# Kernel tuning notes

Measured on AMD Instinct MI355X. Metric: run time of the kernel, lower is better.

## Reference

```python
import jax, jax.numpy as jnp
import numpy as np

B, C, D = 32768, 1000, 512
ALPHA, BETA = 1.0, 1.0
TEMPERATURE = 0.1


def setup_inputs() -> dict:
    key = jax.random.key(0)
    k1, k2, k3, k4 = jax.random.split(key, 4)
    return {
        "features_front": jax.random.normal(k1, (B, D), dtype=jnp.float32),
        "logits": jax.random.normal(k2, (B, C), dtype=jnp.float32),
        "labels": jax.random.randint(k3, (B,), 0, C, dtype=jnp.int64),
        "text_prototype": jax.random.normal(k4, (C, D), dtype=jnp.float32),
    }


def reference(features_front, logits, labels, text_prototype):
    num_class = text_prototype.shape[0]

    # F.cross_entropy (mean reduction)
    logp = jax.nn.log_softmax(logits, axis=-1)
    loss_ce = -jnp.mean(jnp.take_along_axis(logp, labels[:, None], axis=1)[:, 0])

    # F.normalize(prototypes, dim=1)
    norm = jnp.linalg.norm(text_prototype, axis=1, keepdims=True)
    prototypes = text_prototype / jnp.maximum(norm, 1e-12)

    # supervised contrastive term against class prototypes
    feat_dot_prototype = (features_front @ prototypes.T) / TEMPERATURE  # [B, C]
    logits_max = jax.lax.stop_gradient(jnp.max(feat_dot_prototype, axis=1, keepdims=True))
    lg = feat_dot_prototype - logits_max
    log_prob = lg - jnp.log(jnp.sum(jnp.exp(lg), axis=1, keepdims=True))
    mask = (labels[:, None] == jnp.arange(num_class)[None, :]).astype(log_prob.dtype)
    mean_log_prob_pos = jnp.sum(mask * log_prob, axis=1)
    simloss = -jnp.mean(mean_log_prob_pos)

    # prototype repulsion: sum_{i != j} exp(p_i . p_j) == masked exp-sum of Gram matrix
    gram = prototypes @ prototypes.T  # [C, C]
    offdiag = 1.0 - jnp.eye(num_class, dtype=gram.dtype)
    textloss = jnp.log(jnp.sum(jnp.exp(gram) * offdiag)) / num_class

    return ALPHA * simloss + BETA * loss_ce + textloss
```

## Files before the change

kernel.cpp:

```cpp
#include <hip/hip_runtime.h>
#include <math.h>

#define NB 32768
#define NC 1000
#define ND 512
#define NTILES 63
#define LOG2E 1.4426950408889634f
#define LN2 0.6931471805599453f
#define S2 14.426950408889634f
#define NBUCKET 64

typedef __attribute__((ext_vector_type(8))) short short8;
typedef __attribute__((ext_vector_type(4))) float f32x4;

__device__ __forceinline__ float fexp2(float x) {
    float r; asm("v_exp_f32 %0, %1" : "=v"(r) : "v"(x)); return r;
}
__device__ __forceinline__ float flog2(float x) {
    float r; asm("v_log_f32 %0, %1" : "=v"(r) : "v"(x)); return r;
}
__device__ __forceinline__ unsigned short bf16_rne(float f) {
    unsigned int u = __builtin_bit_cast(unsigned int, f);
    u += 0x7FFFu + ((u >> 16) & 1u);
    return (unsigned short)(u >> 16);
}
__device__ __forceinline__ short8 pack8f(float4 a, float4 b) {
    short8 s;
    s[0] = (short)bf16_rne(a.x); s[1] = (short)bf16_rne(a.y);
    s[2] = (short)bf16_rne(a.z); s[3] = (short)bf16_rne(a.w);
    s[4] = (short)bf16_rne(b.x); s[5] = (short)bf16_rne(b.y);
    s[6] = (short)bf16_rne(b.z); s[7] = (short)bf16_rne(b.w);
    return s;
}

__global__ __launch_bounds__(256) void norm_protos(const float* __restrict__ pro,
                                                   unsigned short* __restrict__ pbf) {
    const int row = blockIdx.x, t = threadIdx.x;
    const int tile = row >> 4, r = row & 15;
    const int kk = t >> 4, g = (t >> 2) & 3, slot = t & 3;
    unsigned int* dst = (unsigned int*)pbf +
        ((size_t)tile * 1024 + kk * 64 + g * 16 + r) * 4 + slot;
    if (row >= NC) { *dst = 0u; return; }
    const float* rp = pro + (size_t)row * ND;
    const float x0 = rp[2 * t], x1 = rp[2 * t + 1];
    float ss = x0 * x0 + x1 * x1;
#pragma unroll
    for (int o = 1; o < 64; o <<= 1) ss += __shfl_xor(ss, o, 64);
    __shared__ float part[4];
    if ((t & 63) == 0) part[t >> 6] = ss;
    __syncthreads();
    const float nrm = sqrtf(part[0] + part[1] + part[2] + part[3]);
    const float sc = 1.0f / fmaxf(nrm, 1e-12f);
    *dst = (unsigned int)bf16_rne(x0 * sc) | ((unsigned int)bf16_rne(x1 * sc) << 16);
}

#define TILE_BODY(P, CT)                                                            \
    do {                                                                            \
        f32x4 a0 = {0.f, 0.f, 0.f, 0.f}, a1 = {0.f, 0.f, 0.f, 0.f};                \
        _Pragma("unroll")                                                           \
        for (int kk = 0; kk < 16; ++kk) {                                           \
            a0 = __builtin_amdgcn_mfma_f32_16x16x32_bf16(P[kk], bf0[kk], a0, 0, 0, 0); \
            a1 = __builtin_amdgcn_mfma_f32_16x16x32_bf16(P[kk], bf1[kk], a1, 0, 0, 0); \
        }                                                                           \
        const int cbase = (CT) * 16 + g * 4;                                        \
        {                                                                           \
            float x[4];                                                            \
            _Pragma("unroll")                                                       \
            for (int rI = 0; rI < 4; ++rI) {                                        \
                const float v = a0[rI] * S2;                                        \
                x[rI] = (cbase + rI < NC) ? v : -INFINITY;                          \
                lv0 += (cbase + rI == lab0) ? v : 0.f;                              \
            }                                                                       \
            const float tmax = fmaxf(fmaxf(x[0], x[1]), fmaxf(x[2], x[3]));         \
            const float mn = fmaxf(m0, tmax);                                       \
            ls0 *= fexp2(m0 - mn);                                                  \
            m0 = mn;                                                                \
            ls0 += fexp2(x[0] - mn) + fexp2(x[1] - mn) + fexp2(x[2] - mn) + fexp2(x[3] - mn); \
        }                                                                           \
        {                                                                           \
            float x[4];                                                            \
            _Pragma("unroll")                                                       \
            for (int rI = 0; rI < 4; ++rI) {                                        \
                const float v = a1[rI] * S2;                                        \
                x[rI] = (cbase + rI < NC) ? v : -INFINITY;                          \
                lv1 += (cbase + rI == lab1) ? v : 0.f;                              \
            }                                                                       \
            const float tmax = fmaxf(fmaxf(x[0], x[1]), fmaxf(x[2], x[3]));         \
            const float mn = fmaxf(m1, tmax);                                       \
            ls1 *= fexp2(m1 - mn);                                                  \
            m1 = mn;                                                                \
            ls1 += fexp2(x[0] - mn) + fexp2(x[1] - mn) + fexp2(x[2] - mn) + fexp2(x[3] - mn); \
        }                                                                           \
    } while (0)

__global__ __launch_bounds__(256, 1) void main_kernel(const float* __restrict__ feat,
                                                      const float* __restrict__ logits,
                                                      const int* __restrict__ labels,
                                                      const unsigned short* __restrict__ pbf,
                                                      float* __restrict__ buckets) {
    __shared__ float wsum[4], wsumce[4];
    const int t = threadIdx.x;
    const int wid = t >> 6, lane = t & 63;
    const int r16 = lane & 15, g = lane >> 4;
    const int rowbase = blockIdx.x * 128 + wid * 32;
    const short8* frag = (const short8*)pbf;

    short8 PA[16], PB[16];
#pragma unroll
    for (int k = 0; k < 16; ++k) PA[k] = frag[k * 64 + lane];

    short8 bf0[16], bf1[16];
    {
        const float* f0 = feat + (size_t)(rowbase + r16) * ND + 8 * g;
        const float* f1 = f0 + 16 * ND;
#pragma unroll
        for (int kk = 0; kk < 16; ++kk) {
            bf0[kk] = pack8f(*(const float4*)(f0 + 32 * kk), *(const float4*)(f0 + 32 * kk + 4));
            bf1[kk] = pack8f(*(const float4*)(f1 + 32 * kk), *(const float4*)(f1 + 32 * kk + 4));
        }
    }
    int lab0 = labels[rowbase + r16];
    int lab1 = labels[rowbase + 16 + r16];
    lab0 = lab0 < 0 ? 0 : (lab0 > NC - 1 ? NC - 1 : lab0);
    lab1 = lab1 < 0 ? 0 : (lab1 > NC - 1 ? NC - 1 : lab1);

    float m0 = -INFINITY, ls0 = 0.f, lv0 = 0.f;
    float m1 = -INFINITY, ls1 = 0.f, lv1 = 0.f;

#pragma unroll 1
    for (int ct = 0; ct < 62; ct += 2) {
#pragma unroll
        for (int k = 0; k < 16; ++k) PB[k] = frag[(ct + 1) * 1024 + k * 64 + lane];
        TILE_BODY(PA, ct);
#pragma unroll
        for (int k = 0; k < 16; ++k) PA[k] = frag[(ct + 2) * 1024 + k * 64 + lane];
        TILE_BODY(PB, ct + 1);
        __syncthreads();
    }
    TILE_BODY(PA, 62);

#pragma unroll
    for (int o = 16; o <= 32; o <<= 1) {
        {
            const float mo = __shfl_xor(m0, o, 64), lo = __shfl_xor(ls0, o, 64);
            lv0 += __shfl_xor(lv0, o, 64);
            const float mm = fmaxf(m0, mo);
            ls0 = ls0 * fexp2(m0 - mm) + lo * fexp2(mo - mm);
            m0 = mm;
        }
        {
            const float mo = __shfl_xor(m1, o, 64), lo = __shfl_xor(ls1, o, 64);
            lv1 += __shfl_xor(lv1, o, 64);
            const float mm = fmaxf(m1, mo);
            ls1 = ls1 * fexp2(m1 - mm) + lo * fexp2(mo - mm);
            m1 = mm;
        }
    }
    const float row0 = (m0 + flog2(ls0) - lv0) * LN2;
    const float row1 = (m1 + flog2(ls1) - lv1) * LN2;
    float mine = (row0 + row1) * (1.0f / (4.0f * (float)NB));
#pragma unroll
    for (int o = 1; o < 64; o <<= 1) mine += __shfl_xor(mine, o, 64);

    const int q4 = lane >> 4, l16 = lane & 15;
    float localce = 0.f;
#pragma unroll 1
    for (int i = 0; i < 8; ++i) {
        const int row = rowbase + 4 * i + q4;
        const float* rp = logits + (size_t)row * NC;
        const float4* rp4 = (const float4*)rp;
        float4 xs[16];
#pragma unroll
        for (int j = 0; j < 15; ++j) {
            const float4 v = rp4[l16 + 16 * j];
            xs[j].x = v.x * LOG2E; xs[j].y = v.y * LOG2E;
            xs[j].z = v.z * LOG2E; xs[j].w = v.w * LOG2E;
        }
        if (l16 < 10) {
            const float4 v = rp4[l16 + 240];
            xs[15].x = v.x * LOG2E; xs[15].y = v.y * LOG2E;
            xs[15].z = v.z * LOG2E; xs[15].w = v.w * LOG2E;
        } else {
            xs[15].x = xs[15].y = xs[15].z = xs[15].w = -INFINITY;
        }
        float m = -INFINITY;
#pragma unroll
        for (int j = 0; j < 16; ++j)
            m = fmaxf(m, fmaxf(fmaxf(xs[j].x, xs[j].y), fmaxf(xs[j].z, xs[j].w)));
#pragma unroll
        for (int o = 1; o <= 8; o <<= 1) m = fmaxf(m, __shfl_xor(m, o, 64));
        float s = 0.f;
#pragma unroll
        for (int j = 0; j < 16; ++j)
            s += fexp2(xs[j].x - m) + fexp2(xs[j].y - m) +
                 fexp2(xs[j].z - m) + fexp2(xs[j].w - m);
#pragma unroll
        for (int o = 1; o <= 8; o <<= 1) s += __shfl_xor(s, o, 64);
        if (l16 == 0) {
            int lab = labels[row];
            lab = lab < 0 ? 0 : (lab > NC - 1 ? NC - 1 : lab);
            localce += (m + flog2(s)) * LN2 - rp[lab];
        }
    }

#pragma unroll
    for (int o = 1; o < 64; o <<= 1) localce += __shfl_xor(localce, o, 64);

    if (lane == 0) { wsum[wid] = mine; wsumce[wid] = localce; }
    __syncthreads();
    if (t == 0) {
        const int b = (blockIdx.x & (NBUCKET - 1)) * 16;
        atomicAdd(buckets + b, wsum[0] + wsum[1] + wsum[2] + wsum[3]);
        atomicAdd(buckets + 1024 + b,
                  (wsumce[0] + wsumce[1] + wsumce[2] + wsumce[3]) * (1.0f / (float)NB));
    }
}

__global__ __launch_bounds__(256) void gram_kernel(const unsigned short* __restrict__ pbf,
                                                   float* __restrict__ buckets) {
    __shared__ float wsum[4];
    const int t = threadIdx.x;
    const int wid = t >> 6, lane = t & 63;
    const int r16 = lane & 15, g = lane >> 4;
    const int ct = blockIdx.y;
    const int btile = blockIdx.x * 4 + wid;
    const int irow = btile * 16 + r16;
    const short8* frag = (const short8*)pbf;

    short8 af[16], bfr[16];
#pragma unroll
    for (int kk = 0; kk < 16; ++kk) {
        af[kk] = frag[(size_t)ct * 1024 + kk * 64 + lane];
        bfr[kk] = frag[(size_t)btile * 1024 + kk * 64 + lane];
    }
    f32x4 dacc = {0.f, 0.f, 0.f, 0.f};
#pragma unroll
    for (int kk = 0; kk < 16; ++kk)
        dacc = __builtin_amdgcn_mfma_f32_16x16x32_bf16(af[kk], bfr[kk], dacc, 0, 0, 0);

    float s = 0.f;
    if (irow < NC) {
        const int cbase = ct * 16 + g * 4;
#pragma unroll
        for (int rI = 0; rI < 4; ++rI) {
            const int j = cbase + rI;
            if (j < NC && j != irow) s += fexp2(dacc[rI] * LOG2E);
        }
    }
#pragma unroll
    for (int o = 1; o < 64; o <<= 1) s += __shfl_xor(s, o, 64);
    if (lane == 0) wsum[wid] = s;
    __syncthreads();
    if (t == 0)
        atomicAdd(buckets + ((blockIdx.x + 16 * blockIdx.y) & (NBUCKET - 1)) * 16,
                  wsum[0] + wsum[1] + wsum[2] + wsum[3]);
}

__global__ void combine_kernel(const float* __restrict__ a, float* __restrict__ out) {
    const int t = threadIdx.x;
    float s = a[t * 16], c = a[1024 + t * 16], gr = a[2048 + t * 16];
#pragma unroll
    for (int o = 1; o < 64; o <<= 1) {
        s += __shfl_xor(s, o, 64);
        c += __shfl_xor(c, o, 64);
        gr += __shfl_xor(gr, o, 64);
    }
    if (t == 0) out[0] = s + c + logf(gr) * (1.0f / (float)NC);
}

extern "C" void kernel_launch(void* const* d_in, const int* in_sizes, int n_in,
                              void* d_out, int out_size, void* d_ws, size_t ws_size,
                              hipStream_t stream) {
    const float* feat   = (const float*)d_in[0];
    const float* logits = (const float*)d_in[1];
    const int*   labels = (const int*)d_in[2];
    const float* pro    = (const float*)d_in[3];
    float* out = (float*)d_out;

    float* acc = (float*)d_ws;
    unsigned short* pbf = (unsigned short*)((char*)d_ws + 16384);

    hipMemsetAsync(d_ws, 0, 3072 * sizeof(float), stream);
    hipLaunchKernelGGL(norm_protos,    dim3(1024),     dim3(256), 0, stream, pro, pbf);
    hipLaunchKernelGGL(main_kernel,    dim3(NB / 128), dim3(256), 0, stream, feat, logits, labels, pbf, acc);
    hipLaunchKernelGGL(gram_kernel,    dim3(16, 63),   dim3(256), 0, stream, pbf, acc + 2048);
    hipLaunchKernelGGL(combine_kernel, dim3(1),        dim3(64),  0, stream, acc, out);
}
```

Before: 94.89 us.

## Halve rows per wave, double grid, and split MFMA K-accumulation chain

Each wave now handles 16 feature rows instead of 32, and the grid doubles to NB/64 blocks. The MFMA reduction over K is split into two independent accumulators that are summed before the online softmax, giving more instruction-level parallelism. The per-iteration block barrier is removed. The intent is better occupancy and latency hiding across CUs. In exchange, each prototype fragment is reused across half as many rows, so L2 traffic for prototypes doubles.

```diff
diff --git a/kernel.cpp b/kernel.cpp
--- a/kernel.cpp
+++ b/kernel.cpp
@@ -56,41 +56,25 @@
 
 #define TILE_BODY(P, CT)                                                            \
     do {                                                                            \
-        f32x4 a0 = {0.f, 0.f, 0.f, 0.f}, a1 = {0.f, 0.f, 0.f, 0.f};                \
+        f32x4 aE = {0.f, 0.f, 0.f, 0.f}, aO = {0.f, 0.f, 0.f, 0.f};                \
         _Pragma("unroll")                                                           \
-        for (int kk = 0; kk < 16; ++kk) {                                           \
-            a0 = __builtin_amdgcn_mfma_f32_16x16x32_bf16(P[kk], bf0[kk], a0, 0, 0, 0); \
-            a1 = __builtin_amdgcn_mfma_f32_16x16x32_bf16(P[kk], bf1[kk], a1, 0, 0, 0); \
+        for (int kk = 0; kk < 8; ++kk) {                                            \
+            aE = __builtin_amdgcn_mfma_f32_16x16x32_bf16(P[kk], bf[kk], aE, 0, 0, 0);       \
+            aO = __builtin_amdgcn_mfma_f32_16x16x32_bf16(P[8 + kk], bf[8 + kk], aO, 0, 0, 0); \
         }                                                                           \
         const int cbase = (CT) * 16 + g * 4;                                        \
-        {                                                                           \
-            float x[4];                                                            \
-            _Pragma("unroll")                                                       \
-            for (int rI = 0; rI < 4; ++rI) {                                        \
-                const float v = a0[rI] * S2;                                        \
-                x[rI] = (cbase + rI < NC) ? v : -INFINITY;                          \
-                lv0 += (cbase + rI == lab0) ? v : 0.f;                              \
-            }                                                                       \
-            const float tmax = fmaxf(fmaxf(x[0], x[1]), fmaxf(x[2], x[3]));         \
-            const float mn = fmaxf(m0, tmax);                                       \
-            ls0 *= fexp2(m0 - mn);                                                  \
-            m0 = mn;                                                                \
-            ls0 += fexp2(x[0] - mn) + fexp2(x[1] - mn) + fexp2(x[2] - mn) + fexp2(x[3] - mn); \
+        float x[4];                                                                 \
+        _Pragma("unroll")                                                           \
+        for (int rI = 0; rI < 4; ++rI) {                                            \
+            const float v = (aE[rI] + aO[rI]) * S2;                                 \
+            x[rI] = (cbase + rI < NC) ? v : -INFINITY;    \
+            lv0 += (cbase + rI == lab0) ? v : 0.f;                                  \
         }                                                                           \
-        {                                                                           \
-            float x[4];                                                            \
-            _Pragma("unroll")                                                       \
-            for (int rI = 0; rI < 4; ++rI) {                                        \
-                const float v = a1[rI] * S2;                                        \
-                x[rI] = (cbase + rI < NC) ? v : -INFINITY;                          \
-                lv1 += (cbase + rI == lab1) ? v : 0.f;                              \
-            }                                                                       \
-            const float tmax = fmaxf(fmaxf(x[0], x[1]), fmaxf(x[2], x[3]));         \
-            const float mn = fmaxf(m1, tmax);                                       \
-            ls1 *= fexp2(m1 - mn);                                                  \
-            m1 = mn;                                                                \
-            ls1 += fexp2(x[0] - mn) + fexp2(x[1] - mn) + fexp2(x[2] - mn) + fexp2(x[3] - mn); \
-        }                                                                           \
+        const float tmax = fmaxf(fmaxf(x[0], x[1]), fmaxf(x[2], x[3]));             \
+        const float mn = fmaxf(m0, tmax);                                           \
+        ls0 *= fexp2(m0 - mn);              \
+        m0 = mn;                                                                    \
+        ls0 += fexp2(x[0] - mn) + fexp2(x[1] - mn) + fexp2(x[2] - mn) + fexp2(x[3] - mn); \
     } while (0)
 
 __global__ __launch_bounds__(256, 1) void main_kernel(const float* __restrict__ feat,
@@ -102,30 +86,24 @@
     const int t = threadIdx.x;
     const int wid = t >> 6, lane = t & 63;
     const int r16 = lane & 15, g = lane >> 4;
-    const int rowbase = blockIdx.x * 128 + wid * 32;
+    const int rowbase = blockIdx.x * 64 + wid * 16;
     const short8* frag = (const short8*)pbf;
 
     short8 PA[16], PB[16];
 #pragma unroll
     for (int k = 0; k < 16; ++k) PA[k] = frag[k * 64 + lane];
 
-    short8 bf0[16], bf1[16];
+    short8 bf[16];
     {
         const float* f0 = feat + (size_t)(rowbase + r16) * ND + 8 * g;
-        const float* f1 = f0 + 16 * ND;
-#pragma unroll
-        for (int kk = 0; kk < 16; ++kk) {
-            bf0[kk] = pack8f(*(const float4*)(f0 + 32 * kk), *(const float4*)(f0 + 32 * kk + 4));
-            bf1[kk] = pack8f(*(const float4*)(f1 + 32 * kk), *(const float4*)(f1 + 32 * kk + 4));
-        }
+#pragma unroll
+        for (int kk = 0; kk < 16; ++kk)
+            bf[kk] = pack8f(*(const float4*)(f0 + 32 * kk), *(const float4*)(f0 + 32 * kk + 4));
     }
     int lab0 = labels[rowbase + r16];
-    int lab1 = labels[rowbase + 16 + r16];
     lab0 = lab0 < 0 ? 0 : (lab0 > NC - 1 ? NC - 1 : lab0);
-    lab1 = lab1 < 0 ? 0 : (lab1 > NC - 1 ? NC - 1 : lab1);
 
     float m0 = -INFINITY, ls0 = 0.f, lv0 = 0.f;
-    float m1 = -INFINITY, ls1 = 0.f, lv1 = 0.f;
 
 #pragma unroll 1
     for (int ct = 0; ct < 62; ct += 2) {
@@ -135,37 +113,26 @@
 #pragma unroll
         for (int k = 0; k < 16; ++k) PA[k] = frag[(ct + 2) * 1024 + k * 64 + lane];
         TILE_BODY(PB, ct + 1);
-        __syncthreads();
     }
     TILE_BODY(PA, 62);
 
 #pragma unroll
     for (int o = 16; o <= 32; o <<= 1) {
-        {
-            const float mo = __shfl_xor(m0, o, 64), lo = __shfl_xor(ls0, o, 64);
-            lv0 += __shfl_xor(lv0, o, 64);
-            const float mm = fmaxf(m0, mo);
-            ls0 = ls0 * fexp2(m0 - mm) + lo * fexp2(mo - mm);
-            m0 = mm;
-        }
-        {
-            const float mo = __shfl_xor(m1, o, 64), lo = __shfl_xor(ls1, o, 64);
-            lv1 += __shfl_xor(lv1, o, 64);
-            const float mm = fmaxf(m1, mo);
-            ls1 = ls1 * fexp2(m1 - mm) + lo * fexp2(mo - mm);
-            m1 = mm;
-        }
+        const float mo = __shfl_xor(m0, o, 64), lo = __shfl_xor(ls0, o, 64);
+        lv0 += __shfl_xor(lv0, o, 64);
+        const float mm = fmaxf(m0, mo);
+        ls0 = ls0 * fexp2(m0 - mm) + lo * fexp2(mo - mm);
+        m0 = mm;
     }
     const float row0 = (m0 + flog2(ls0) - lv0) * LN2;
-    const float row1 = (m1 + flog2(ls1) - lv1) * LN2;
-    float mine = (row0 + row1) * (1.0f / (4.0f * (float)NB));
+    float mine = row0 * (1.0f / (4.0f * (float)NB));
 #pragma unroll
     for (int o = 1; o < 64; o <<= 1) mine += __shfl_xor(mine, o, 64);
 
     const int q4 = lane >> 4, l16 = lane & 15;
     float localce = 0.f;
 #pragma unroll 1
-    for (int i = 0; i < 8; ++i) {
+    for (int i = 0; i < 4; ++i) {
         const int row = rowbase + 4 * i + q4;
         const float* rp = logits + (size_t)row * NC;
         const float4* rp4 = (const float4*)rp;
@@ -281,8 +248,8 @@
     unsigned short* pbf = (unsigned short*)((char*)d_ws + 16384);
 
     hipMemsetAsync(d_ws, 0, 3072 * sizeof(float), stream);
-    hipLaunchKernelGGL(norm_protos,    dim3(1024),     dim3(256), 0, stream, pro, pbf);
-    hipLaunchKernelGGL(main_kernel,    dim3(NB / 128), dim3(256), 0, stream, feat, logits, labels, pbf, acc);
-    hipLaunchKernelGGL(gram_kernel,    dim3(16, 63),   dim3(256), 0, stream, pbf, acc + 2048);
-    hipLaunchKernelGGL(combine_kernel, dim3(1),        dim3(64),  0, stream, acc, out);
-}
+    hipLaunchKernelGGL(norm_protos,    dim3(1024),    dim3(256), 0, stream, pro, pbf);
+    hipLaunchKernelGGL(main_kernel,    dim3(NB / 64), dim3(256), 0, stream, feat, logits, labels, pbf, acc);
+    hipLaunchKernelGGL(gram_kernel,    dim3(16, 63),  dim3(256), 0, stream, pbf, acc + 2048);
+    hipLaunchKernelGGL(combine_kernel, dim3(1),       dim3(64),  0, stream, acc, out);
+}
```

After: 103.3 us. 1.09x slower.
